# Kernel optimization log

Measured on AMD Instinct MI355X. Metric: run time of the kernel, lower is better.

## Reference

```python
import jax, jax.numpy as jnp
import numpy as np

B, T, C = 4, 2048, 1024
HEADS = 16
HEAD_DIM = C // HEADS
WINDOW = 256


def setup_inputs() -> dict:
    key = jax.random.key(0)
    k1, k2, k3 = jax.random.split(key, 3)
    x = jax.random.normal(k1, (B, T, C), dtype=jnp.float32)
    # torch nn.Linear weights: [out_features, in_features]; scale like kaiming-uniform-ish
    W_qkv = jax.random.normal(k2, (3 * C, C), dtype=jnp.float32) * (1.0 / np.sqrt(C))
    W_proj = jax.random.normal(k3, (C, C), dtype=jnp.float32) * (1.0 / np.sqrt(C))
    return {"x": x, "W_qkv": W_qkv, "W_proj": W_proj}


def reference(x, W_qkv, W_proj):
    b, t, c = x.shape
    h, d = HEADS, HEAD_DIM
    qkv = x @ W_qkv.T  # [b,t,3c]
    q, k, v = jnp.split(qkv, 3, axis=-1)
    q = q.reshape(b, t, h, d).transpose(0, 2, 1, 3)  # [b,h,t,d]
    k = k.reshape(b, t, h, d).transpose(0, 2, 1, 3)
    v = v.reshape(b, t, h, d).transpose(0, 2, 1, 3)
    scale = 1.0 / jnp.sqrt(jnp.asarray(d, dtype=q.dtype))
    scores = jnp.einsum('bhqd,bhkd->bhqk', q, k) * scale  # [b,h,t,t]
    i = jnp.arange(t)[:, None]
    j = jnp.arange(t)[None, :]
    mask = (j <= i) & (j > i - WINDOW)  # sliding-window causal band
    scores = jnp.where(mask, scores, -jnp.inf)
    attn = jax.nn.softmax(scores, axis=-1)
    y = jnp.einsum('bhqk,bhkd->bhqd', attn, v)  # [b,h,t,d]
    y = y.transpose(0, 2, 1, 3).reshape(b, t, c)
    return y @ W_proj.T
```

## Files before the change

kernel.cpp:

```cpp
#include <hip/hip_runtime.h>
#include <hip/hip_bf16.h>
#include <math.h>

#define BB 4
#define TT 2048
#define CC 1024
#define HH 16
#define DD 64
#define WW 256
#define MM (BB*TT)
#define NX (MM*CC)
#define NQ (3*CC*CC)
#define NP (CC*CC)

typedef __bf16 bf16x8 __attribute__((ext_vector_type(8)));
typedef __bf16 bf16x4 __attribute__((ext_vector_type(4)));
typedef float  f32x4  __attribute__((ext_vector_type(4)));

__device__ __forceinline__ void async_cp16(const void* g, void* l) {
  __builtin_amdgcn_global_load_lds(
      (const __attribute__((address_space(1))) void*)g,
      (__attribute__((address_space(3))) void*)l, 16, 0, 0);
}

__device__ __forceinline__ unsigned short f2bf(float v) {
  __hip_bfloat16 h = __float2bfloat16(v);
  return *(unsigned short*)&h;
}

__global__ __launch_bounds__(256)
void prep(const float* __restrict__ x,
          const float* __restrict__ wq,
          const float* __restrict__ wp,
          __hip_bfloat16* __restrict__ wdst,
          unsigned short* __restrict__ Apk) {
  const int p = blockIdx.x;
  const int tid = threadIdx.x;
  if (p < 4096) {
    int i = (p * 256 + tid) * 4;
    const float* src; int off;
    if (i < NQ) { src = wq; off = i; }
    else        { src = wp; off = i - NQ; }
    float4 v = *(const float4*)(src + off);
    wdst[i + 0] = __float2bfloat16(v.x);
    wdst[i + 1] = __float2bfloat16(v.y);
    wdst[i + 2] = __float2bfloat16(v.z);
    wdst[i + 3] = __float2bfloat16(v.w);
    return;
  }
  __shared__ __align__(16) unsigned short tile[64 * 72];
  const int pid = p - 4096;
  const int bm = pid & 127;
  const int bk = pid >> 7;
  const int tr = tid >> 4;
  const int tc = (tid & 15) * 4;
#pragma unroll
  for (int i = 0; i < 4; i++) {
    int row = i * 16 + tr;
    float4 v = *(const float4*)&x[(size_t)(bm * 64 + row) * 1024 + bk * 64 + tc];
    tile[row * 72 + tc + 0] = f2bf(v.x);
    tile[row * 72 + tc + 1] = f2bf(v.y);
    tile[row * 72 + tc + 2] = f2bf(v.z);
    tile[row * 72 + tc + 3] = f2bf(v.w);
  }
  __syncthreads();
  const int w = tid >> 6, lane = tid & 63;
  const int quad = lane >> 4, l15 = lane & 15;
#pragma unroll
  for (int f = 0; f < 2; f++) {
    bf16x8 fr = *(const bf16x8*)&tile[(w * 16 + l15) * 72 + f * 32 + quad * 8];
    *(bf16x8*)&Apk[(((size_t)(bm * 4 + w) * 32) + bk * 2 + f) * 512 + lane * 8] = fr;
  }
}

__global__ __launch_bounds__(256, 2)
void gemm_qkv(const unsigned short* __restrict__ Apk,
              const unsigned short* __restrict__ Bw,
              unsigned short* __restrict__ Qh,
              unsigned short* __restrict__ Kh,
              unsigned short* __restrict__ Vh) {
  __shared__ __align__(16) unsigned short Bs0[16 * 1024];
  __shared__ __align__(16) unsigned short Bs1[16 * 1024];

  const int id   = blockIdx.x;
  const int xcd  = id & 7;
  const int slot = id >> 3;
  const int mblk = slot / 3;
  const int nloc = slot % 3;
  const int n0 = (xcd * 3 + nloc) * 128;
  const int m0 = mblk * 256;

  const int tid  = threadIdx.x;
  const int w    = tid >> 6;
  const int lane = tid & 63;
  const int quad = lane >> 4;
  const int l15  = lane & 15;

  f32x4 acc[4][8];
#pragma unroll
  for (int i = 0; i < 4; i++)
#pragma unroll
    for (int j = 0; j < 8; j++) acc[i][j] = (f32x4)0.0f;

  const unsigned short* abase =
      Apk + ((size_t)((m0 >> 4) + w * 4) * 32) * 512 + lane * 8;

  auto stageB = [&](int k0, unsigned short* bs) {
#pragma unroll
    for (int i = 0; i < 8; i++) {
      int idx  = w + 4 * i;
      int kc   = idx >> 1;
      int half = idx & 1;
      async_cp16(Bw + (size_t)(n0 + half * 64 + lane) * 1024 + k0 + kc * 8,
                 &bs[kc * 1024 + half * 512]);
    }
  };

  bf16x8 Af[2][4];
  auto loadA = [&](int g, bf16x8* fr) {
#pragma unroll
    for (int tm = 0; tm < 4; tm++)
      fr[tm] = *(const bf16x8*)(abase + ((size_t)(tm * 32 + g)) * 512);
  };

  loadA(0, Af[0]);
  stageB(0, Bs0);
  __syncthreads();

#pragma unroll
  for (int s = 0; s < 8; s++) {
    const unsigned short* bs = (s & 1) ? Bs1 : Bs0;
    if (s + 1 < 8) stageB((s + 1) * 128, (s & 1) ? Bs0 : Bs1);
#pragma unroll
    for (int sub = 0; sub < 4; sub++) {
      const int g = s * 4 + sub;
      if (g + 1 < 32) loadA(g + 1, Af[(g + 1) & 1]);
      const bf16x8* af = Af[g & 1];
#pragma unroll
      for (int tn = 0; tn < 8; tn++) {
        bf16x8 bfv = *(const bf16x8*)
            &bs[(sub * 4 + quad) * 1024 + (tn * 16 + l15) * 8];
#pragma unroll
        for (int tm = 0; tm < 4; tm++)
          acc[tm][tn] = __builtin_amdgcn_mfma_f32_16x16x32_bf16(
              af[tm], bfv, acc[tm][tn], 0, 0, 0);
      }
    }
    __syncthreads();
  }

#pragma unroll
  for (int tm = 0; tm < 4; tm++)
#pragma unroll
    for (int tn = 0; tn < 8; tn++) {
      int colb = n0 + tn * 16;
      int t3 = colb >> 10;
      int hh = (colb >> 6) & 15;
      int dd = (colb & 63) + l15;
      unsigned short* dst = (t3 == 0) ? Qh : ((t3 == 1) ? Kh : Vh);
      float sc = (t3 == 0) ? 0.125f : 1.0f;
#pragma unroll
      for (int r = 0; r < 4; r++) {
        int row = m0 + w * 64 + tm * 16 + quad * 4 + r;
        int b = row >> 11, tt = row & 2047;
        dst[((size_t)((b * 16 + hh) * 2048 + tt)) * 64 + dd] =
            f2bf(acc[tm][tn][r] * sc);
      }
    }
}

__global__ __launch_bounds__(256, 2)
void gemm_proj(const unsigned short* __restrict__ Apk,
               const unsigned short* __restrict__ Bw,
               float* __restrict__ Co) {
  __shared__ __align__(16) unsigned short Bs0[16 * 1024];
  __shared__ __align__(16) unsigned short Bs1[16 * 1024];

  const int id = blockIdx.x;
  const int n0 = (id & 7) * 128;
  const int m0 = (id >> 3) * 128;

  const int tid  = threadIdx.x;
  const int w    = tid >> 6;
  const int lane = tid & 63;
  const int quad = lane >> 4;
  const int l15  = lane & 15;

  f32x4 acc[2][8];
#pragma unroll
  for (int i = 0; i < 2; i++)
#pragma unroll
    for (int j = 0; j < 8; j++) acc[i][j] = (f32x4)0.0f;

  const unsigned short* abase =
      Apk + ((size_t)((m0 >> 4) + w * 2) * 32) * 512 + lane * 8;

  auto stageB = [&](int k0, unsigned short* bs) {
#pragma unroll
    for (int i = 0; i < 8; i++) {
      int idx  = w + 4 * i;
      int kc   = idx >> 1;
      int half = idx & 1;
      async_cp16(Bw + (size_t)(n0 + half * 64 + lane) * 1024 + k0 + kc * 8,
                 &bs[kc * 1024 + half * 512]);
    }
  };

  bf16x8 Af[2][2];
  auto loadA = [&](int g, bf16x8* fr) {
#pragma unroll
    for (int tm = 0; tm < 2; tm++)
      fr[tm] = *(const bf16x8*)(abase + ((size_t)(tm * 32 + g)) * 512);
  };

  loadA(0, Af[0]);
  stageB(0, Bs0);
  __syncthreads();

#pragma unroll
  for (int s = 0; s < 8; s++) {
    const unsigned short* bs = (s & 1) ? Bs1 : Bs0;
    if (s + 1 < 8) stageB((s + 1) * 128, (s & 1) ? Bs0 : Bs1);
#pragma unroll
    for (int sub = 0; sub < 4; sub++) {
      const int g = s * 4 + sub;
      if (g + 1 < 32) loadA(g + 1, Af[(g + 1) & 1]);
      const bf16x8* af = Af[g & 1];
#pragma unroll
      for (int tn = 0; tn < 8; tn++) {
        bf16x8 bfv = *(const bf16x8*)
            &bs[(sub * 4 + quad) * 1024 + (tn * 16 + l15) * 8];
#pragma unroll
        for (int tm = 0; tm < 2; tm++)
          acc[tm][tn] = __builtin_amdgcn_mfma_f32_16x16x32_bf16(
              af[tm], bfv, acc[tm][tn], 0, 0, 0);
      }
    }
    __syncthreads();
  }

#pragma unroll
  for (int tm = 0; tm < 2; tm++)
#pragma unroll
    for (int tn = 0; tn < 8; tn++)
#pragma unroll
      for (int r = 0; r < 4; r++) {
        int row = m0 + w * 32 + tm * 16 + quad * 4 + r;
        int col = n0 + tn * 16 + l15;
        Co[(size_t)row * 1024 + col] = acc[tm][tn][r];
      }
}

__global__ __launch_bounds__(256)
void transpose_v(const unsigned short* __restrict__ Vh,
                 unsigned short* __restrict__ Vt) {
  __shared__ __align__(16) unsigned short tile[64 * 72];
  const int tid = threadIdx.x;
  const int tc = blockIdx.x, bh = blockIdx.y;
  const unsigned short* src = Vh + ((size_t)bh * 2048 + (size_t)tc * 64) * 64;
  for (int i = tid; i < 512; i += 256) {
    int r = i >> 3, ds = (i & 7) * 8;
    *(uint4*)&tile[r * 72 + ds] = *(const uint4*)&src[(size_t)r * 64 + ds];
  }
  __syncthreads();
  unsigned short* dst = Vt + (size_t)(bh * 32 + tc) * 4096;
  for (int i = tid; i < 512; i += 256) {
    int d = i >> 3, ts = (i & 7) * 8;
    unsigned int w0 = tile[(ts + 0) * 72 + d] | ((unsigned int)tile[(ts + 1) * 72 + d] << 16);
    unsigned int w1 = tile[(ts + 2) * 72 + d] | ((unsigned int)tile[(ts + 3) * 72 + d] << 16);
    unsigned int w2 = tile[(ts + 4) * 72 + d] | ((unsigned int)tile[(ts + 5) * 72 + d] << 16);
    unsigned int w3 = tile[(ts + 6) * 72 + d] | ((unsigned int)tile[(ts + 7) * 72 + d] << 16);
    uint4 o; o.x = w0; o.y = w1; o.z = w2; o.w = w3;
    *(uint4*)&dst[(size_t)d * 64 + ts] = o;
  }
}

__global__ __launch_bounds__(256, 2)
void attn_mfma(const unsigned short* __restrict__ Qh,
               const unsigned short* __restrict__ Kh,
               const unsigned short* __restrict__ Vt,
               unsigned short* __restrict__ Ypk) {
  __shared__ __align__(16) unsigned short SH[40960];

  const int tid  = threadIdx.x;
  const int w    = tid >> 6;
  const int lane = tid & 63;
  const int quad = lane >> 4;
  const int l15  = lane & 15;
  const int q0 = blockIdx.x * 64;
  const int bh = blockIdx.y;

  const int c0 = (q0 >= 256) ? 0 : (4 - (q0 >> 6));

  const unsigned short* Qg = Qh + ((size_t)bh * 2048 + q0) * 64;
  bf16x8 Qf[2];
#pragma unroll
  for (int fs = 0; fs < 2; fs++)
    Qf[fs] = *(const bf16x8*)(Qg + (w * 16 + l15) * 64 + fs * 32 + quad * 8);

  const unsigned short* Kg = Kh + (size_t)bh * 2048 * 64;
  const unsigned short* Vg = Vt + (size_t)bh * 32 * 4096;
  for (int ch = c0; ch < 5; ch++) {
    int sc = q0 - 256 + ch * 64;
#pragma unroll
    for (int i = 0; i < 2; i++) {
      int kc = w * 2 + i;
      async_cp16(Kg + (size_t)(sc + lane) * 64 + kc * 8,
                 &SH[ch * 4096 + kc * 512]);
      async_cp16(Vg + (size_t)(sc >> 6) * 4096 + lane * 64 + kc * 8,
                 &SH[20480 + ch * 4096 + kc * 512]);
    }
  }
  __syncthreads();

  f32x4 S[5][4];
#pragma unroll
  for (int ch = 0; ch < 5; ch++)
#pragma unroll
    for (int tn = 0; tn < 4; tn++) S[ch][tn] = (f32x4)0.0f;

#pragma unroll
  for (int ch = 0; ch < 5; ch++) {
    if (ch < c0) continue;
#pragma unroll
    for (int ks = 0; ks < 2; ks++) {
      int kc = ks * 4 + quad;
#pragma unroll
      for (int tn = 0; tn < 4; tn++) {
        bf16x8 bk = *(const bf16x8*)
            &SH[ch * 4096 + kc * 512 + (tn * 16 + l15) * 8];
        S[ch][tn] = __builtin_amdgcn_mfma_f32_16x16x32_bf16(
            Qf[ks], bk, S[ch][tn], 0, 0, 0);
      }
    }
  }

  const int qb = q0 + w * 16 + quad * 4;
  if (c0 == 0) {
#pragma unroll
    for (int tn = 0; tn < 4; tn++) {
      int j = q0 - 256 + tn * 16 + l15;
#pragma unroll
      for (int r = 0; r < 4; r++)
        if (qb + r > j + (WW - 1)) S[0][tn][r] = -__builtin_inff();
    }
  }
#pragma unroll
  for (int tn = 0; tn < 4; tn++) {
    int j = q0 + tn * 16 + l15;
#pragma unroll
    for (int r = 0; r < 4; r++)
      if (j > qb + r) S[4][tn][r] = -__builtin_inff();
  }

  float mrow[4], lrow[4];
#pragma unroll
  for (int r = 0; r < 4; r++) mrow[r] = -__builtin_inff();
#pragma unroll
  for (int ch = 0; ch < 5; ch++) {
    if (ch < c0) continue;
#pragma unroll
    for (int tn = 0; tn < 4; tn++)
#pragma unroll
      for (int r = 0; r < 4; r++)
        mrow[r] = fmaxf(mrow[r], S[ch][tn][r]);
  }
#pragma unroll
  for (int off = 1; off < 16; off <<= 1)
#pragma unroll
    for (int r = 0; r < 4; r++)
      mrow[r] = fmaxf(mrow[r], __shfl_xor(mrow[r], off));

#pragma unroll
  for (int r = 0; r < 4; r++) lrow[r] = 0.0f;
#pragma unroll
  for (int ch = 0; ch < 5; ch++) {
    if (ch < c0) continue;
#pragma unroll
    for (int tn = 0; tn < 4; tn++)
#pragma unroll
      for (int r = 0; r < 4; r++) {
        float e = __expf(S[ch][tn][r] - mrow[r]);
        S[ch][tn][r] = e;
        lrow[r] += e;
      }
  }
#pragma unroll
  for (int off = 1; off < 16; off <<= 1)
#pragma unroll
    for (int r = 0; r < 4; r++) lrow[r] += __shfl_xor(lrow[r], off);

  __syncthreads();

  f32x4 Oacc[4];
#pragma unroll
  for (int td = 0; td < 4; td++) Oacc[td] = (f32x4)0.0f;

#pragma unroll
  for (int ch = 0; ch < 5; ch++) {
    if (ch < c0) continue;
    unsigned short* Ps = SH + (ch & 1) * 4608;
#pragma unroll
    for (int tn = 0; tn < 4; tn++)
#pragma unroll
      for (int r = 0; r < 4; r++)
        Ps[(w * 16 + quad * 4 + r) * 68 + tn * 16 + l15] = f2bf(S[ch][tn][r]);
    asm volatile("s_waitcnt lgkmcnt(0)" ::: "memory");
#pragma unroll
    for (int ks = 0; ks < 2; ks++) {
      int off = (w * 16 + l15) * 68 + ks * 32 + quad * 8;
      bf16x4 plo = *(const bf16x4*)&Ps[off];
      bf16x4 phi = *(const bf16x4*)&Ps[off + 4];
      bf16x8 ap = __builtin_shufflevector(plo, phi, 0, 1, 2, 3, 4, 5, 6, 7);
      int kc = ks * 4 + quad;
#pragma unroll
      for (int td = 0; td < 4; td++) {
        bf16x8 bv = *(const bf16x8*)
            &SH[20480 + ch * 4096 + kc * 512 + (td * 16 + l15) * 8];
        Oacc[td] = __builtin_amdgcn_mfma_f32_16x16x32_bf16(
            ap, bv, Oacc[td], 0, 0, 0);
      }
    }
  }

  const int b = bh >> 4, h = bh & 15;
  float inv[4];
#pragma unroll
  for (int r = 0; r < 4; r++) inv[r] = 1.0f / lrow[r];
  unsigned short* Ot = SH + 10240;
#pragma unroll
  for (int td = 0; td < 4; td++)
#pragma unroll
    for (int r = 0; r < 4; r++)
      Ot[(w * 16 + quad * 4 + r) * 72 + td * 16 + l15] =
          f2bf(Oacc[td][r] * inv[r]);
  asm volatile("s_waitcnt lgkmcnt(0)" ::: "memory");
  const size_t rt = (size_t)((b * 2048 + q0) >> 4) + w;
#pragma unroll
  for (int f = 0; f < 2; f++) {
    bf16x8 fr = *(const bf16x8*)&Ot[(w * 16 + l15) * 72 + f * 32 + quad * 8];
    *(bf16x8*)&Ypk[(rt * 32 + h * 2 + f) * 512 + lane * 8] = fr;
  }
}

extern "C" void kernel_launch(void* const* d_in, const int* in_sizes, int n_in,
                              void* d_out, int out_size, void* d_ws, size_t ws_size,
                              hipStream_t stream) {
  const float* x     = (const float*)d_in[0];
  const float* wqkv  = (const float*)d_in[1];
  const float* wproj = (const float*)d_in[2];
  float* out = (float*)d_out;

  char* ws = (char*)d_ws;
  unsigned short* apk    = (unsigned short*)(ws);
  unsigned short* vtb    = (unsigned short*)(ws);
  unsigned short* wqkvb  = (unsigned short*)(ws + (size_t)16 * 1024 * 1024);
  unsigned short* wprojb = (unsigned short*)(ws + (size_t)22 * 1024 * 1024);
  unsigned short* qh     = (unsigned short*)(ws + (size_t)24 * 1024 * 1024);
  unsigned short* kh     = (unsigned short*)(ws + (size_t)40 * 1024 * 1024);
  unsigned short* vh     = (unsigned short*)(ws + (size_t)56 * 1024 * 1024);
  unsigned short* ypk    = (unsigned short*)(ws + (size_t)72 * 1024 * 1024);

  prep<<<4096 + 2048, 256, 0, stream>>>(
      x, wqkv, wproj, (__hip_bfloat16*)wqkvb, apk);

  gemm_qkv<<<768, 256, 0, stream>>>(apk, wqkvb, qh, kh, vh);

  transpose_v<<<dim3(32, 64), 256, 0, stream>>>(vh, vtb);

  attn_mfma<<<dim3(TT / 64, BB * HH), 256, 0, stream>>>(
      qh, kh, vtb, ypk);

  gemm_proj<<<512, 256, 0, stream>>>(ypk, wprojb, out);
}
```

Measured before the change: 238.7 us.

## Fuse V transpose into QKV GEMM epilogue and deepen A-fragment prefetch

The QKV GEMM epilogue now writes V tiles directly in the transposed per-64-token layout, staging them through the freed LDS B buffers, so the separate transpose_v kernel is removed. This saves one launch plus a full write and read of V through global memory. Both GEMMs also move from double- to triple-buffered A fragments (prefetch distance two), which hides more global load latency at the cost of extra registers. The LDS reuse depends on the final __syncthreads of the main loop and on per-warp private staging regions.

```diff
diff --git a/kernel.cpp b/kernel.cpp
--- a/kernel.cpp
+++ b/kernel.cpp
@@ -78,7 +78,7 @@
               const unsigned short* __restrict__ Bw,
               unsigned short* __restrict__ Qh,
               unsigned short* __restrict__ Kh,
-              unsigned short* __restrict__ Vh) {
+              unsigned short* __restrict__ Vt) {
   __shared__ __align__(16) unsigned short Bs0[16 * 1024];
   __shared__ __align__(16) unsigned short Bs1[16 * 1024];
 
@@ -116,7 +116,7 @@
     }
   };
 
-  bf16x8 Af[2][4];
+  bf16x8 Af[3][4];
   auto loadA = [&](int g, bf16x8* fr) {
 #pragma unroll
     for (int tm = 0; tm < 4; tm++)
@@ -124,6 +124,7 @@
   };
 
   loadA(0, Af[0]);
+  loadA(1, Af[1]);
   stageB(0, Bs0);
   __syncthreads();
 
@@ -134,8 +135,8 @@
 #pragma unroll
     for (int sub = 0; sub < 4; sub++) {
       const int g = s * 4 + sub;
-      if (g + 1 < 32) loadA(g + 1, Af[(g + 1) & 1]);
-      const bf16x8* af = Af[g & 1];
+      if (g + 2 < 32) loadA(g + 2, Af[(g + 2) % 3]);
+      const bf16x8* af = Af[g % 3];
 #pragma unroll
       for (int tn = 0; tn < 8; tn++) {
         bf16x8 bfv = *(const bf16x8*)
@@ -149,24 +150,52 @@
     __syncthreads();
   }
 
-#pragma unroll
-  for (int tm = 0; tm < 4; tm++)
-#pragma unroll
-    for (int tn = 0; tn < 8; tn++) {
-      int colb = n0 + tn * 16;
-      int t3 = colb >> 10;
-      int hh = (colb >> 6) & 15;
-      int dd = (colb & 63) + l15;
-      unsigned short* dst = (t3 == 0) ? Qh : ((t3 == 1) ? Kh : Vh);
-      float sc = (t3 == 0) ? 0.125f : 1.0f;
-#pragma unroll
-      for (int r = 0; r < 4; r++) {
-        int row = m0 + w * 64 + tm * 16 + quad * 4 + r;
-        int b = row >> 11, tt = row & 2047;
-        dst[((size_t)((b * 16 + hh) * 2048 + tt)) * 64 + dd] =
-            f2bf(acc[tm][tn][r] * sc);
-      }
-    }
+  const int t3 = n0 >> 10;
+  if (t3 < 2) {
+    unsigned short* dst0 = (t3 == 0) ? Qh : Kh;
+    const float sc = (t3 == 0) ? 0.125f : 1.0f;
+#pragma unroll
+    for (int tm = 0; tm < 4; tm++)
+#pragma unroll
+      for (int tn = 0; tn < 8; tn++) {
+        int colb = n0 + tn * 16;
+        int hh = (colb >> 6) & 15;
+        int dd = (colb & 63) + l15;
+#pragma unroll
+        for (int r = 0; r < 4; r++) {
+          int row = m0 + w * 64 + tm * 16 + quad * 4 + r;
+          int b = row >> 11, tt = row & 2047;
+          dst0[((size_t)((b * 16 + hh) * 2048 + tt)) * 64 + dd] =
+              f2bf(acc[tm][tn][r] * sc);
+        }
+      }
+  } else {
+    unsigned short* T = (w < 3) ? (Bs0 + w * 4608) : Bs1;
+    const int b    = (m0 + w * 64) >> 11;
+    const int tc_g = ((m0 & 2047) >> 6) + w;
+    const int h0   = (n0 >> 6) & 15;
+#pragma unroll
+    for (int hp = 0; hp < 2; hp++) {
+#pragma unroll
+      for (int tnl = 0; tnl < 4; tnl++)
+#pragma unroll
+        for (int tm = 0; tm < 4; tm++)
+#pragma unroll
+          for (int r = 0; r < 4; r++)
+            T[(tnl * 16 + l15) * 72 + tm * 16 + quad * 4 + r] =
+                f2bf(acc[tm][hp * 4 + tnl][r]);
+      asm volatile("s_waitcnt lgkmcnt(0)" ::: "memory");
+      const size_t base =
+          ((size_t)((b * 16 + h0 + hp) * 32 + tc_g)) * 4096;
+#pragma unroll
+      for (int i = 0; i < 8; i++) {
+        int d   = i * 8 + (lane >> 3);
+        int tin = (lane & 7) * 8;
+        bf16x8 v = *(const bf16x8*)&T[d * 72 + tin];
+        *(bf16x8*)&Vt[base + (size_t)d * 64 + tin] = v;
+      }
+    }
+  }
 }
 
 __global__ __launch_bounds__(256, 2)
@@ -206,7 +235,7 @@
     }
   };
 
-  bf16x8 Af[2][2];
+  bf16x8 Af[3][2];
   auto loadA = [&](int g, bf16x8* fr) {
 #pragma unroll
     for (int tm = 0; tm < 2; tm++)
@@ -214,6 +243,7 @@
   };
 
   loadA(0, Af[0]);
+  loadA(1, Af[1]);
   stageB(0, Bs0);
   __syncthreads();
 
@@ -224,8 +254,8 @@
 #pragma unroll
     for (int sub = 0; sub < 4; sub++) {
       const int g = s * 4 + sub;
-      if (g + 1 < 32) loadA(g + 1, Af[(g + 1) & 1]);
-      const bf16x8* af = Af[g & 1];
+      if (g + 2 < 32) loadA(g + 2, Af[(g + 2) % 3]);
+      const bf16x8* af = Af[g % 3];
 #pragma unroll
       for (int tn = 0; tn < 8; tn++) {
         bf16x8 bfv = *(const bf16x8*)
@@ -249,30 +279,6 @@
         int col = n0 + tn * 16 + l15;
         Co[(size_t)row * 1024 + col] = acc[tm][tn][r];
       }
-}
-
-__global__ __launch_bounds__(256)
-void transpose_v(const unsigned short* __restrict__ Vh,
-                 unsigned short* __restrict__ Vt) {
-  __shared__ __align__(16) unsigned short tile[64 * 72];
-  const int tid = threadIdx.x;
-  const int tc = blockIdx.x, bh = blockIdx.y;
-  const unsigned short* src = Vh + ((size_t)bh * 2048 + (size_t)tc * 64) * 64;
-  for (int i = tid; i < 512; i += 256) {
-    int r = i >> 3, ds = (i & 7) * 8;
-    *(uint4*)&tile[r * 72 + ds] = *(const uint4*)&src[(size_t)r * 64 + ds];
-  }
-  __syncthreads();
-  unsigned short* dst = Vt + (size_t)(bh * 32 + tc) * 4096;
-  for (int i = tid; i < 512; i += 256) {
-    int d = i >> 3, ts = (i & 7) * 8;
-    unsigned int w0 = tile[(ts + 0) * 72 + d] | ((unsigned int)tile[(ts + 1) * 72 + d] << 16);
-    unsigned int w1 = tile[(ts + 2) * 72 + d] | ((unsigned int)tile[(ts + 3) * 72 + d] << 16);
-    unsigned int w2 = tile[(ts + 4) * 72 + d] | ((unsigned int)tile[(ts + 5) * 72 + d] << 16);
-    unsigned int w3 = tile[(ts + 6) * 72 + d] | ((unsigned int)tile[(ts + 7) * 72 + d] << 16);
-    uint4 o; o.x = w0; o.y = w1; o.z = w2; o.w = w3;
-    *(uint4*)&dst[(size_t)d * 64 + ts] = o;
-  }
 }
 
 __global__ __launch_bounds__(256, 2)
@@ -453,23 +459,20 @@
 
   char* ws = (char*)d_ws;
   unsigned short* apk    = (unsigned short*)(ws);
-  unsigned short* vtb    = (unsigned short*)(ws);
   unsigned short* wqkvb  = (unsigned short*)(ws + (size_t)16 * 1024 * 1024);
   unsigned short* wprojb = (unsigned short*)(ws + (size_t)22 * 1024 * 1024);
   unsigned short* qh     = (unsigned short*)(ws + (size_t)24 * 1024 * 1024);
   unsigned short* kh     = (unsigned short*)(ws + (size_t)40 * 1024 * 1024);
-  unsigned short* vh     = (unsigned short*)(ws + (size_t)56 * 1024 * 1024);
+  unsigned short* vt     = (unsigned short*)(ws + (size_t)56 * 1024 * 1024);
   unsigned short* ypk    = (unsigned short*)(ws + (size_t)72 * 1024 * 1024);
 
   prep<<<4096 + 2048, 256, 0, stream>>>(
       x, wqkv, wproj, (__hip_bfloat16*)wqkvb, apk);
 
-  gemm_qkv<<<768, 256, 0, stream>>>(apk, wqkvb, qh, kh, vh);
-
-  transpose_v<<<dim3(32, 64), 256, 0, stream>>>(vh, vtb);
+  gemm_qkv<<<768, 256, 0, stream>>>(apk, wqkvb, qh, kh, vt);
 
   attn_mfma<<<dim3(TT / 64, BB * HH), 256, 0, stream>>>(
-      qh, kh, vtb, ypk);
+      qh, kh, vt, ypk);
 
   gemm_proj<<<512, 256, 0, stream>>>(ypk, wprojb, out);
 }
```

After: 230.8 us. 3.3% less time.
